# Kernel tuning notes

Hardware: AMD Instinct MI355X
Metric: run time of the kernel (lower is better)

## Reference

```python
import jax, jax.numpy as jnp
import numpy as np

DROPOUT_P = 0.1
DROPOUT_KEY = jax.random.key(42)


def setup_inputs() -> dict:
    key = jax.random.key(0)
    kq, kk, kv = jax.random.split(key, 3)
    B, S, H, D = 2, 2048, 16, 64
    query = jax.random.normal(kq, (B, S, H, D), dtype=jnp.float32)
    k_in = jax.random.normal(kk, (B, S, H, D), dtype=jnp.float32)
    value = jax.random.normal(kv, (B, S, H, D), dtype=jnp.float32)
    inv_scale_factor = jnp.asarray(8.0, dtype=jnp.float32)  # sqrt(head_dim)
    return {"query": query, "key": k_in, "value": value,
            "inv_scale_factor": inv_scale_factor}


def reference(query, key, value, inv_scale_factor):
    # permute(0,2,1,3): [B, S, H, D] -> [B, H, S, D]
    q = jnp.transpose(query, (0, 2, 1, 3))
    k = jnp.transpose(key, (0, 2, 1, 3))
    v = jnp.transpose(value, (0, 2, 1, 3))
    # scores: [B, H, S, S]
    scores = jnp.einsum("bhsd,bhtd->bhst", q, k) / inv_scale_factor
    attn = jax.nn.softmax(scores, axis=-1)
    # dropout (train mode, inverted scaling) with a fixed key
    keep = jax.random.bernoulli(DROPOUT_KEY, 1.0 - DROPOUT_P, attn.shape)
    attn = jnp.where(keep, attn / (1.0 - DROPOUT_P), 0.0)
    # output: [B, H, S, D]
    return jnp.einsum("bhst,bhtd->bhsd", attn, v)
```

## Files before the change

kernel.cpp:

```cpp
#include <hip/hip_runtime.h>
#include <hip/hip_bf16.h>
#include <stdint.h>

typedef __attribute__((ext_vector_type(8))) short short8;
typedef __attribute__((ext_vector_type(4))) float f32x4;
typedef __attribute__((ext_vector_type(4))) uint32_t u32x4;
typedef __attribute__((ext_vector_type(2))) uint32_t u32x2;

#define KEEP_TH 0xE6666600u

__device__ __forceinline__ uint32_t pack2bf(float a, float b) {
  uint16_t lo = __builtin_bit_cast(uint16_t, __float2bfloat16(a));
  uint16_t hi = __builtin_bit_cast(uint16_t, __float2bfloat16(b));
  return (uint32_t)lo | ((uint32_t)hi << 16);
}

__device__ __forceinline__ uint32_t tf_bits(uint32_t x1pre) {
  uint32_t x1 = x1pre;
  uint32_t x0 = x1;
  x1 = __builtin_rotateleft32(x1, 13) ^ x0;
#define R(r) { x0 += x1; x1 = __builtin_rotateleft32(x1, (r)) ^ x0; }
  R(15) R(26) R(6)
  x0 += 42u;          x1 += 0x1BD11BF0u + 1u;
  R(17) R(29) R(16) R(24)
  x0 += 0x1BD11BF0u;  x1 += 2u;
  R(13) R(15) R(26) R(6)
                      x1 += 42u + 3u;
  R(17) R(29) R(16) R(24)
  x0 += 42u;          x1 += 0x1BD11BF0u + 4u;
  R(13) R(15) R(26) R(6)
  x0 += 0x1BD11BF0u;  x1 += 5u;
#undef R
  return x0 ^ x1;
}


__global__ __launch_bounds__(256, 4)
void attn_dropout_kernel(const float* __restrict__ Qg, const float* __restrict__ Kg,
                         const float* __restrict__ Vg, const float* __restrict__ invs,
                         float* __restrict__ Out) {
  __shared__ __align__(16) uint32_t KbF[512 * 4];
  __shared__ __align__(16) uint32_t VtF[512 * 4];
  __shared__ __align__(16) uint32_t PlF[512 * 4];

  const int tid = threadIdx.x;
  const int w = tid >> 6;
  const int l = tid & 63;
  const int e = l & 15;
  const int g = l >> 4;

  const int n  = blockIdx.x;
  const int bh = (n & 7) * 4 + ((n >> 3) & 3);
  const int b  = bh >> 4;
  const int h  = bh & 15;
  const int qc = n >> 5;
  const int qbase = qc * 64;

  const float c = 1.4426950408889634f / invs[0];
  const int sq = qbase + w * 16 + e;

  short8 qf[2];
#pragma unroll
  for (int kc = 0; kc < 2; ++kc) {
    const float* qp = Qg + (((b * 2048 + sq) * 16 + h) * 64 + kc * 32 + 8 * g);
    f32x4 q0 = *(const f32x4*)qp;
    f32x4 q1 = *(const f32x4*)(qp + 4);
    u32x4 u;
    u.x = pack2bf(q0.x * c, q0.y * c);
    u.y = pack2bf(q0.z * c, q0.w * c);
    u.z = pack2bf(q1.x * c, q1.y * c);
    u.w = pack2bf(q1.z * c, q1.w * c);
    qf[kc] = __builtin_bit_cast(short8, u);
  }

  f32x4 acc[4];
#pragma unroll
  for (int dt = 0; dt < 4; ++dt) acc[dt] = (f32x4){0.f, 0.f, 0.f, 0.f};
  float lsum = 0.f;

  const uint32_t fb = ((uint32_t)b << 26) | ((uint32_t)h << 22) | ((uint32_t)sq << 11);

  const int s_e = tid & 15, s_g = (tid >> 4) & 3, s_kc = (tid >> 6) & 1, s_T = tid >> 7;
  const int v_e = tid & 15, v_gk = (tid >> 4) & 7, v_dt = tid >> 7;

  for (int tile = 0; tile < 32; ++tile) {
    const int t0 = tile * 64;
    __syncthreads();
#pragma unroll
    for (int r2 = 0; r2 < 2; ++r2) {
      int Tk = s_T + 2 * r2;
      const float* p = Kg + (((b * 2048 + t0 + Tk * 16 + s_e) * 16 + h) * 64 + s_kc * 32 + 8 * s_g);
      f32x4 a0 = *(const f32x4*)p;
      f32x4 a1 = *(const f32x4*)(p + 4);
      u32x4 u;
      u.x = pack2bf(a0.x, a0.y);
      u.y = pack2bf(a0.z, a0.w);
      u.z = pack2bf(a1.x, a1.y);
      u.w = pack2bf(a1.z, a1.w);
      *(u32x4*)&KbF[(((Tk * 2 + s_kc) * 4 + s_g) * 16 + s_e) * 4] = u;
    }
#pragma unroll
    for (int r2 = 0; r2 < 2; ++r2) {
      int dt = v_dt + 2 * r2;
      int d = dt * 16 + v_e;
      const float* p = Vg + (((b * 2048 + t0 + 8 * v_gk) * 16 + h) * 64 + d);
      float vv[8];
#pragma unroll
      for (int r = 0; r < 8; ++r) vv[r] = p[r * 1024];
      u32x4 u;
      u.x = pack2bf(vv[0], vv[1]);
      u.y = pack2bf(vv[2], vv[3]);
      u.z = pack2bf(vv[4], vv[5]);
      u.w = pack2bf(vv[6], vv[7]);
      *(u32x4*)&VtF[((dt * 8 + v_gk) * 16 + v_e) * 4] = u;
    }
    __syncthreads();

#pragma unroll
    for (int Tk = 0; Tk < 4; ++Tk) {
      u32x4 ku0 = *(const u32x4*)&KbF[(((Tk * 2 + 0) * 4 + g) * 16 + e) * 4];
      u32x4 ku1 = *(const u32x4*)&KbF[(((Tk * 2 + 1) * 4 + g) * 16 + e) * 4];
      f32x4 sacc = (f32x4){0.f, 0.f, 0.f, 0.f};
      sacc = __builtin_amdgcn_mfma_f32_16x16x32_bf16(__builtin_bit_cast(short8, ku0), qf[0], sacc, 0, 0, 0);
      sacc = __builtin_amdgcn_mfma_f32_16x16x32_bf16(__builtin_bit_cast(short8, ku1), qf[1], sacc, 0, 0, 0);
      const uint32_t jT = fb + (uint32_t)(t0 + 16 * Tk + 4 * g + 42);
      float pm[4];
#pragma unroll
      for (int r = 0; r < 4; ++r) {
        uint32_t bits = tf_bits(jT + (uint32_t)r);
        float pv = __builtin_amdgcn_exp2f(sacc[r]);
        lsum += pv;
        pm[r] = (bits < KEEP_TH) ? pv : 0.f;
      }
      int gp = 2 * Tk + (g >> 1);
      u32x2 pw;
      pw.x = pack2bf(pm[0], pm[1]);
      pw.y = pack2bf(pm[2], pm[3]);
      *(u32x2*)&PlF[((w * 8 + gp) * 16 + e) * 4 + 2 * (g & 1)] = pw;
    }
    asm volatile("" ::: "memory");

#pragma unroll
    for (int kk = 0; kk < 2; ++kk) {
      u32x4 pu = *(const u32x4*)&PlF[((w * 8 + g + 4 * kk) * 16 + e) * 4];
      short8 pf = __builtin_bit_cast(short8, pu);
#pragma unroll
      for (int dt = 0; dt < 4; ++dt) {
        u32x4 vu = *(const u32x4*)&VtF[((dt * 8 + g + 4 * kk) * 16 + e) * 4];
        acc[dt] = __builtin_amdgcn_mfma_f32_16x16x32_bf16(pf, __builtin_bit_cast(short8, vu), acc[dt], 0, 0, 0);
      }
    }
  }

  float L = lsum;
  L += __shfl_xor(L, 16);
  L += __shfl_xor(L, 32);
  float rinv = 1.0f / (0.9f * L);
  float rr[4];
#pragma unroll
  for (int r = 0; r < 4; ++r) rr[r] = __shfl(rinv, 4 * g + r);
#pragma unroll
  for (int dt = 0; dt < 4; ++dt)
#pragma unroll
    for (int r = 0; r < 4; ++r) {
      int s = qbase + w * 16 + 4 * g + r;
      Out[(((b * 16 + h) * 2048 + s) * 64) + dt * 16 + e] = acc[dt][r] * rr[r];
    }
}

extern "C" void kernel_launch(void* const* d_in, const int* in_sizes, int n_in,
                              void* d_out, int out_size, void* d_ws, size_t ws_size,
                              hipStream_t stream) {
  const float* q  = (const float*)d_in[0];
  const float* k  = (const float*)d_in[1];
  const float* v  = (const float*)d_in[2];
  const float* sc = (const float*)d_in[3];
  float* out = (float*)d_out;
  (void)d_ws; (void)ws_size; (void)in_sizes; (void)n_in; (void)out_size;
  attn_dropout_kernel<<<dim3(1024), dim3(256), 0, stream>>>(q, k, v, sc, out);
}
```

Measured before the change: 295.7 us.

## Prefetch next K/V tile into registers and use packed bf16 convert

Loads the next tile's K and V values into registers right after the LDS barrier, so global loads overlap with the QK/softmax/PV compute of the current tile. It replaces the scalar two-step bf16 conversion with the v_cvt_pk_bf16_f32 instruction. It also splits the row-sum accumulator into four independent partials. This raises register usage, which could reduce occupancy or cause spills.

```diff
diff --git a/kernel.cpp b/kernel.cpp
--- a/kernel.cpp
+++ b/kernel.cpp
@@ -9,10 +9,10 @@
 
 #define KEEP_TH 0xE6666600u
 
-__device__ __forceinline__ uint32_t pack2bf(float a, float b) {
-  uint16_t lo = __builtin_bit_cast(uint16_t, __float2bfloat16(a));
-  uint16_t hi = __builtin_bit_cast(uint16_t, __float2bfloat16(b));
-  return (uint32_t)lo | ((uint32_t)hi << 16);
+__device__ __forceinline__ uint32_t pkbf(float lo, float hi) {
+  uint32_t r;
+  asm("v_cvt_pk_bf16_f32 %0, %1, %2" : "=v"(r) : "v"(lo), "v"(hi));
+  return r;
 }
 
 __device__ __forceinline__ uint32_t tf_bits(uint32_t x1pre) {
@@ -66,55 +66,75 @@
     f32x4 q0 = *(const f32x4*)qp;
     f32x4 q1 = *(const f32x4*)(qp + 4);
     u32x4 u;
-    u.x = pack2bf(q0.x * c, q0.y * c);
-    u.y = pack2bf(q0.z * c, q0.w * c);
-    u.z = pack2bf(q1.x * c, q1.y * c);
-    u.w = pack2bf(q1.z * c, q1.w * c);
+    u.x = pkbf(q0.x * c, q0.y * c);
+    u.y = pkbf(q0.z * c, q0.w * c);
+    u.z = pkbf(q1.x * c, q1.y * c);
+    u.w = pkbf(q1.z * c, q1.w * c);
     qf[kc] = __builtin_bit_cast(short8, u);
   }
 
   f32x4 acc[4];
 #pragma unroll
   for (int dt = 0; dt < 4; ++dt) acc[dt] = (f32x4){0.f, 0.f, 0.f, 0.f};
-  float lsum = 0.f;
+  float ls[4] = {0.f, 0.f, 0.f, 0.f};
 
   const uint32_t fb = ((uint32_t)b << 26) | ((uint32_t)h << 22) | ((uint32_t)sq << 11);
 
   const int s_e = tid & 15, s_g = (tid >> 4) & 3, s_kc = (tid >> 6) & 1, s_T = tid >> 7;
   const int v_e = tid & 15, v_gk = (tid >> 4) & 7, v_dt = tid >> 7;
+
+  const float* kbase = Kg + (((b * 2048 + s_T * 16 + s_e) * 16 + h) * 64 + s_kc * 32 + 8 * s_g);
+  const float* vbase = Vg + (((b * 2048 + 8 * v_gk) * 16 + h) * 64 + v_dt * 16 + v_e);
+
+  f32x4 kA[2], kB[2];
+  float vR[2][8];
+
+#pragma unroll
+  for (int r2 = 0; r2 < 2; ++r2) {
+    const float* p = kbase + r2 * (32 * 16 * 64);
+    kA[r2] = *(const f32x4*)p;
+    kB[r2] = *(const f32x4*)(p + 4);
+    const float* pv = vbase + r2 * (2 * 16 * 64);
+#pragma unroll
+    for (int r = 0; r < 8; ++r) vR[r2][r] = pv[r * 1024 - r2 * (2 * 16 * 64) + r2 * 32];
+  }
 
   for (int tile = 0; tile < 32; ++tile) {
     const int t0 = tile * 64;
     __syncthreads();
+
 #pragma unroll
     for (int r2 = 0; r2 < 2; ++r2) {
       int Tk = s_T + 2 * r2;
-      const float* p = Kg + (((b * 2048 + t0 + Tk * 16 + s_e) * 16 + h) * 64 + s_kc * 32 + 8 * s_g);
-      f32x4 a0 = *(const f32x4*)p;
-      f32x4 a1 = *(const f32x4*)(p + 4);
       u32x4 u;
-      u.x = pack2bf(a0.x, a0.y);
-      u.y = pack2bf(a0.z, a0.w);
-      u.z = pack2bf(a1.x, a1.y);
-      u.w = pack2bf(a1.z, a1.w);
+      u.x = pkbf(kA[r2].x, kA[r2].y);
+      u.y = pkbf(kA[r2].z, kA[r2].w);
+      u.z = pkbf(kB[r2].x, kB[r2].y);
+      u.w = pkbf(kB[r2].z, kB[r2].w);
       *(u32x4*)&KbF[(((Tk * 2 + s_kc) * 4 + s_g) * 16 + s_e) * 4] = u;
-    }
-#pragma unroll
-    for (int r2 = 0; r2 < 2; ++r2) {
+
       int dt = v_dt + 2 * r2;
-      int d = dt * 16 + v_e;
-      const float* p = Vg + (((b * 2048 + t0 + 8 * v_gk) * 16 + h) * 64 + d);
-      float vv[8];
-#pragma unroll
-      for (int r = 0; r < 8; ++r) vv[r] = p[r * 1024];
-      u32x4 u;
-      u.x = pack2bf(vv[0], vv[1]);
-      u.y = pack2bf(vv[2], vv[3]);
-      u.z = pack2bf(vv[4], vv[5]);
-      u.w = pack2bf(vv[6], vv[7]);
-      *(u32x4*)&VtF[((dt * 8 + v_gk) * 16 + v_e) * 4] = u;
+      u32x4 uv;
+      uv.x = pkbf(vR[r2][0], vR[r2][1]);
+      uv.y = pkbf(vR[r2][2], vR[r2][3]);
+      uv.z = pkbf(vR[r2][4], vR[r2][5]);
+      uv.w = pkbf(vR[r2][6], vR[r2][7]);
+      *(u32x4*)&VtF[((dt * 8 + v_gk) * 16 + v_e) * 4] = uv;
     }
     __syncthreads();
+
+    if (tile + 1 < 32) {
+      const int t1 = (tile + 1) * 64;
+#pragma unroll
+      for (int r2 = 0; r2 < 2; ++r2) {
+        const float* p = kbase + (t1 + r2 * 32) * (16 * 64);
+        kA[r2] = *(const f32x4*)p;
+        kB[r2] = *(const f32x4*)(p + 4);
+        const float* pv = vbase + (t1) * (16 * 64) + r2 * 32;
+#pragma unroll
+        for (int r = 0; r < 8; ++r) vR[r2][r] = pv[r * 1024];
+      }
+    }
 
 #pragma unroll
     for (int Tk = 0; Tk < 4; ++Tk) {
@@ -129,13 +149,13 @@
       for (int r = 0; r < 4; ++r) {
         uint32_t bits = tf_bits(jT + (uint32_t)r);
         float pv = __builtin_amdgcn_exp2f(sacc[r]);
-        lsum += pv;
+        ls[r] += pv;
         pm[r] = (bits < KEEP_TH) ? pv : 0.f;
       }
       int gp = 2 * Tk + (g >> 1);
       u32x2 pw;
-      pw.x = pack2bf(pm[0], pm[1]);
-      pw.y = pack2bf(pm[2], pm[3]);
+      pw.x = pkbf(pm[0], pm[1]);
+      pw.y = pkbf(pm[2], pm[3]);
       *(u32x2*)&PlF[((w * 8 + gp) * 16 + e) * 4 + 2 * (g & 1)] = pw;
     }
     asm volatile("" ::: "memory");
@@ -152,7 +172,7 @@
     }
   }
 
-  float L = lsum;
+  float L = (ls[0] + ls[1]) + (ls[2] + ls[3]);
   L += __shfl_xor(L, 16);
   L += __shfl_xor(L, 32);
   float rinv = 1.0f / (0.9f * L);
```

After: 280.8 us. -5.0%, faster.
